# Kernel optimization log

Measured on AMD Instinct MI355X. Metric: run time of the kernel, lower is better.

The kernel has to match this reference:

```python
import jax, jax.numpy as jnp
import numpy as np
import math

NUM_BUCKETS = 32
MAX_DISTANCE = 128
N_HEADS = 16
D_KV = 64
D_MODEL = 1024


def _relative_position_bucket(relative_position, num_buckets=NUM_BUCKETS, max_distance=MAX_DISTANCE):
    # bidirectional (encoder) variant
    num_buckets = num_buckets // 2
    relative_buckets = (relative_position > 0).astype(jnp.int32) * num_buckets
    relative_position = jnp.abs(relative_position)
    max_exact = num_buckets // 2
    is_small = relative_position < max_exact
    # avoid log(0); masked by is_small anyway
    rp = jnp.maximum(relative_position, 1).astype(jnp.float32)
    rel_if_large = max_exact + (
        jnp.log(rp / max_exact) / math.log(max_distance / max_exact) * (num_buckets - max_exact)
    ).astype(jnp.int32)
    rel_if_large = jnp.minimum(rel_if_large, num_buckets - 1)
    relative_buckets = relative_buckets + jnp.where(is_small, relative_position, rel_if_large)
    return relative_buckets


def compute_bias(rel_bias, q_len, k_len):
    context = jnp.arange(q_len, dtype=jnp.int32)[:, None]
    memory = jnp.arange(k_len, dtype=jnp.int32)[None, :]
    buckets = _relative_position_bucket(memory - context)  # [q,k]
    values = rel_bias[buckets]                              # [q,k,H]
    return jnp.transpose(values, (2, 0, 1))[None]           # [1,H,q,k]


def setup_inputs() -> dict:
    key = jax.random.key(0)
    k1, k2, k3, k4 = jax.random.split(key, 4)
    B, S = 2, 2048
    hidden_states = jax.random.normal(k1, (B, S, D_MODEL), dtype=jnp.float32)
    attention_mask = jnp.ones((B, S), dtype=jnp.int32)
    w_qkv = jax.random.normal(k2, (3 * D_MODEL, D_MODEL), dtype=jnp.float32) * 0.02
    rel_bias = jax.random.normal(k3, (NUM_BUCKETS, N_HEADS), dtype=jnp.float32)
    w_o = jax.random.normal(k4, (D_MODEL, D_MODEL), dtype=jnp.float32) * 0.02
    return {"hidden_states": hidden_states, "attention_mask": attention_mask,
            "w_qkv": w_qkv, "rel_bias": rel_bias, "w_o": w_o}


def reference(hidden_states, attention_mask, w_qkv, rel_bias, w_o):
    B, S, _ = hidden_states.shape
    n, c = N_HEADS, D_KV
    qkv = hidden_states @ w_qkv.T                      # [B,S,3*inner]
    q, k, v = jnp.split(qkv, 3, axis=-1)
    q = q.reshape(B, S, n, c)
    k = k.reshape(B, S, n, c)
    v = v.reshape(B, S, n, c)
    attn_bias = jnp.broadcast_to(compute_bias(rel_bias, S, S), (B, n, S, S))
    mask = attention_mask.reshape(B, 1, 1, S)
    mask_val = jnp.finfo(q.dtype).min
    attn_bias = jnp.where(mask == 0, mask_val, attn_bias)
    attn = jnp.einsum('binc,bjnc->bnij', q, k) + attn_bias   # no 1/sqrt(d) scale in T5
    attn = jax.nn.softmax(attn.astype(jnp.float32), axis=-1).astype(q.dtype)
    x = jnp.einsum('bnij,bjnc->binc', attn, v)
    x = x.reshape(B, S, n * c)
    return x @ w_o.T
```

## Files before the change

### kernel.cpp

```cpp
#include <hip/hip_runtime.h>
#include <stdint.h>

typedef __attribute__((ext_vector_type(4))) float f32x4;
typedef __attribute__((ext_vector_type(8))) short short8;
typedef __attribute__((ext_vector_type(4))) short short4v;
typedef __attribute__((ext_vector_type(2))) unsigned uint2v;

__device__ __forceinline__ short f2bf(float f) {
    union { float f; unsigned u; } x; x.f = f;
    return (short)((x.u + 0x7fffu + ((x.u >> 16) & 1u)) >> 16);
}

__device__ __forceinline__ unsigned cvt_pk_bf16(float lo, float hi) {
    unsigned r;
    asm("v_cvt_pk_bf16_f32 %0, %1, %2" : "=v"(r) : "v"(lo), "v"(hi));
    return r;
}

__device__ __forceinline__ float fexp2(float x) {
#if __has_builtin(__builtin_amdgcn_exp2f)
    return __builtin_amdgcn_exp2f(x);
#else
    return exp2f(x);
#endif
}

#define MFMA16(a, b, c) __builtin_amdgcn_mfma_f32_16x16x32_bf16((a), (b), (c), 0, 0, 0)

__device__ __forceinline__ void gload16(const void* g, void* l) {
    __builtin_amdgcn_global_load_lds((const __attribute__((address_space(1))) void*)g,
                                     (__attribute__((address_space(3))) void*)l, 16, 0, 0);
}

__global__ __launch_bounds__(256) void cast_all(const float* __restrict__ h,
                                                const float* __restrict__ wq,
                                                const float* __restrict__ wo,
                                                short* __restrict__ hb,
                                                short* __restrict__ wqb,
                                                short* __restrict__ wob) {
    int i = blockIdx.x * 256 + threadIdx.x;
    const float* s;
    short* d;
    int j;
    if (i < 524288) { s = h; d = hb; j = i; }
    else if (i < 917504) { s = wq; d = wqb; j = i - 524288; }
    else { s = wo; d = wob; j = i - 917504; }
    float4 a = ((const float4*)s)[j * 2];
    float4 b = ((const float4*)s)[j * 2 + 1];
    short8 o;
    o[0] = f2bf(a.x); o[1] = f2bf(a.y); o[2] = f2bf(a.z); o[3] = f2bf(a.w);
    o[4] = f2bf(b.x); o[5] = f2bf(b.y); o[6] = f2bf(b.z); o[7] = f2bf(b.w);
    ((short8*)d)[j] = o;
}

template <int OUT_BF16, int QSCALE>
__global__ __launch_bounds__(512, 2) void gemm8p(const short* __restrict__ A,
                                                 const short* __restrict__ B,
                                                 void* __restrict__ Cout,
                                                 int M, int N, int K) {
    __shared__ short lds[2][4][8192];
    const int t = threadIdx.x;
    const int l = t & 63, w = t >> 6;
    const int lr = l & 15, lg = l >> 4;
    const int wr = w >> 2, wc = w & 3;
    const int m0 = blockIdx.y * 256, n0 = blockIdx.x * 256;
    const int nt = K >> 6, nh = nt << 2;

    const int sr0 = t >> 2;
    const int scc = ((t & 3) ^ ((sr0 >> 1) & 3)) * 8;
    const short* As0 = A + (size_t)(m0 + sr0) * K + scc;
    const short* As1 = A + (size_t)(m0 + sr0 + 128) * K + scc;
    const short* Bs0 = B + (size_t)(n0 + sr0) * K + scc;
    const short* Bs1 = B + (size_t)(n0 + sr0 + 128) * K + scc;
    short* ldsb = &lds[0][0][0];

    auto stageH = [&](int H) {
        int Tp = H >> 2, pos = H & 3;
        int kb = Tp * 64 + ((pos <= 1) ? 32 : 0);
        short* dst = ldsb + ((Tp & 1) * 4 + pos) * 8192 + t * 8;
        if (pos & 1) {
            gload16(As0 + kb, dst);
            gload16(As1 + kb, dst + 4096);
        } else {
            gload16(Bs0 + kb, dst);
            gload16(Bs1 + kb, dst + 4096);
        }
    };

    int aoff[8], boff[4];
    #pragma unroll
    for (int mi = 0; mi < 8; ++mi) {
        int row = wr * 128 + mi * 16 + lr;
        aoff[mi] = row * 32 + (lg ^ ((row >> 1) & 3)) * 8;
    }
    #pragma unroll
    for (int ni = 0; ni < 4; ++ni) {
        int row = wc * 64 + ni * 16 + lr;
        boff[ni] = row * 32 + (lg ^ ((row >> 1) & 3)) * 8;
    }

    f32x4 acc[8][4] = {};

    for (int H = 0; H < 7; ++H) stageH(H);
    asm volatile("s_waitcnt vmcnt(6)" ::: "memory");
    __builtin_amdgcn_s_barrier();

    for (int T = 0; T < nt; ++T) {
        const short* rbase = ldsb + (T & 1) * 32768;
        const short* B1b = rbase;
        const short* A1b = rbase + 8192;
        const short* B0b = rbase + 16384;
        const short* A0b = rbase + 24576;
        const int Hs = (T << 2) + 7;
        short8 a[4], b[4];

        #pragma unroll
        for (int i = 0; i < 4; ++i) a[i] = *(const short8*)(A1b + aoff[i]);
        #pragma unroll
        for (int i = 0; i < 4; ++i) b[i] = *(const short8*)(B1b + boff[i]);
        if (Hs < nh) stageH(Hs);
        __builtin_amdgcn_sched_barrier(0);
        __builtin_amdgcn_s_barrier();
        asm volatile("s_waitcnt lgkmcnt(0)" ::: "memory");
        __builtin_amdgcn_sched_barrier(0);
        __builtin_amdgcn_s_setprio(1);
        #pragma unroll
        for (int mi = 0; mi < 4; ++mi)
            #pragma unroll
            for (int ni = 0; ni < 4; ++ni)
                acc[mi][ni] = MFMA16(a[mi], b[ni], acc[mi][ni]);
        __builtin_amdgcn_s_setprio(0);
        __builtin_amdgcn_sched_barrier(0);
        __builtin_amdgcn_s_barrier();

        #pragma unroll
        for (int i = 0; i < 4; ++i) a[i] = *(const short8*)(A1b + aoff[4 + i]);
        if (Hs + 1 < nh) stageH(Hs + 1);
        __builtin_amdgcn_sched_barrier(0);
        __builtin_amdgcn_s_barrier();
        asm volatile("s_waitcnt lgkmcnt(0)" ::: "memory");
        __builtin_amdgcn_sched_barrier(0);
        __builtin_amdgcn_s_setprio(1);
        #pragma unroll
        for (int mi = 0; mi < 4; ++mi)
            #pragma unroll
            for (int ni = 0; ni < 4; ++ni)
                acc[4 + mi][ni] = MFMA16(a[mi], b[ni], acc[4 + mi][ni]);
        __builtin_amdgcn_s_setprio(0);
        __builtin_amdgcn_sched_barrier(0);
        __builtin_amdgcn_s_barrier();

        #pragma unroll
        for (int i = 0; i < 4; ++i) a[i] = *(const short8*)(A0b + aoff[i]);
        #pragma unroll
        for (int i = 0; i < 4; ++i) b[i] = *(const short8*)(B0b + boff[i]);
        if (Hs + 2 < nh) stageH(Hs + 2);
        __builtin_amdgcn_sched_barrier(0);
        __builtin_amdgcn_s_barrier();
        asm volatile("s_waitcnt lgkmcnt(0)" ::: "memory");
        __builtin_amdgcn_sched_barrier(0);
        __builtin_amdgcn_s_setprio(1);
        #pragma unroll
        for (int mi = 0; mi < 4; ++mi)
            #pragma unroll
            for (int ni = 0; ni < 4; ++ni)
                acc[mi][ni] = MFMA16(a[mi], b[ni], acc[mi][ni]);
        __builtin_amdgcn_s_setprio(0);
        __builtin_amdgcn_sched_barrier(0);
        __builtin_amdgcn_s_barrier();

        #pragma unroll
        for (int i = 0; i < 4; ++i) a[i] = *(const short8*)(A0b + aoff[4 + i]);
        if (Hs + 3 < nh) stageH(Hs + 3);
        __builtin_amdgcn_sched_barrier(0);
        __builtin_amdgcn_s_barrier();
        asm volatile("s_waitcnt lgkmcnt(0)" ::: "memory");
        __builtin_amdgcn_sched_barrier(0);
        __builtin_amdgcn_s_setprio(1);
        #pragma unroll
        for (int mi = 0; mi < 4; ++mi)
            #pragma unroll
            for (int ni = 0; ni < 4; ++ni)
                acc[4 + mi][ni] = MFMA16(a[mi], b[ni], acc[4 + mi][ni]);
        __builtin_amdgcn_s_setprio(0);
        if (T < nt - 2) {
            asm volatile("s_waitcnt vmcnt(6)" ::: "memory");
        } else if (T == nt - 2) {
            asm volatile("s_waitcnt vmcnt(0)" ::: "memory");
        }
        __builtin_amdgcn_sched_barrier(0);
        __builtin_amdgcn_s_barrier();
    }

    const float qs = (QSCALE && n0 < 1024) ? 1.4426950408889634f : 1.0f;
    #pragma unroll
    for (int mi = 0; mi < 8; ++mi)
        #pragma unroll
        for (int ni = 0; ni < 4; ++ni)
            #pragma unroll
            for (int rr = 0; rr < 4; ++rr) {
                int mm = m0 + wr * 128 + mi * 16 + lg * 4 + rr;
                int nn = n0 + wc * 64 + ni * 16 + lr;
                float v = acc[mi][ni][rr] * qs;
                if (OUT_BF16) ((short*)Cout)[(size_t)mm * N + nn] = f2bf(v);
                else ((float*)Cout)[(size_t)mm * N + nn] = v;
            }
}

template <int OUT_BF16, int QSCALE>
__global__ __launch_bounds__(256) void gemm_bt(const short* __restrict__ A,
                                               const short* __restrict__ B,
                                               void* __restrict__ Cout,
                                               int M, int N, int K) {
    __shared__ short sA[4096];
    __shared__ short sB[4096];
    const int t = threadIdx.x;
    const int l = t & 63, w = t >> 6;
    const int lr = l & 15, lg = l >> 4;
    const int m0 = blockIdx.y * 128, n0 = blockIdx.x * 128;
    const int wm = (w >> 1) * 64, wn = (w & 1) * 64;
    const int c0 = w * 64 + l, c1 = c0 + 256;
    const short* Ap0 = A + (size_t)(m0 + (c0 >> 2)) * K + (c0 & 3) * 8;
    const short* Ap1 = A + (size_t)(m0 + (c1 >> 2)) * K + (c1 & 3) * 8;
    const short* Bp0 = B + (size_t)(n0 + (c0 >> 2)) * K + (c0 & 3) * 8;
    const short* Bp1 = B + (size_t)(n0 + (c1 >> 2)) * K + (c1 & 3) * 8;
    short* lA0 = sA + w * 512;
    short* lA1 = sA + 2048 + w * 512;
    short* lB0 = sB + w * 512;
    short* lB1 = sB + 2048 + w * 512;
    f32x4 acc[4][4] = {};
    for (int k0 = 0; k0 < K; k0 += 32) {
        gload16(Ap0 + k0, lA0);
        gload16(Ap1 + k0, lA1);
        gload16(Bp0 + k0, lB0);
        gload16(Bp1 + k0, lB1);
        __syncthreads();
        short8 af[4], bfr[4];
        #pragma unroll
        for (int m = 0; m < 4; ++m) af[m] = *(const short8*)&sA[(wm + m * 16 + lr) * 32 + lg * 8];
        #pragma unroll
        for (int n = 0; n < 4; ++n) bfr[n] = *(const short8*)&sB[(wn + n * 16 + lr) * 32 + lg * 8];
        #pragma unroll
        for (int m = 0; m < 4; ++m)
            #pragma unroll
            for (int n = 0; n < 4; ++n)
                acc[m][n] = MFMA16(af[m], bfr[n], acc[m][n]);
        __syncthreads();
    }
    const float qs = (QSCALE && n0 < 1024) ? 1.4426950408889634f : 1.0f;
    #pragma unroll
    for (int m = 0; m < 4; ++m)
        #pragma unroll
        for (int n = 0; n < 4; ++n)
            #pragma unroll
            for (int r = 0; r < 4; ++r) {
                int mm = m0 + wm + m * 16 + lg * 4 + r;
                int nn = n0 + wn + n * 16 + lr;
                float v = acc[m][n][r] * qs;
                if (OUT_BF16) ((short*)Cout)[(size_t)mm * N + nn] = f2bf(v);
                else ((float*)Cout)[(size_t)mm * N + nn] = v;
            }
}

__global__ __launch_bounds__(256) void transpose_v(const short* __restrict__ qkv,
                                                   short* __restrict__ vt) {
    __shared__ short T[64][72];
    const int t = threadIdx.x;
    const int s0 = blockIdx.x * 64, bh = blockIdx.y;
    const int b = bh >> 4, h = bh & 15;
    const int rl = t >> 2, cg = (t & 3) * 16;
    const short* src = qkv + (size_t)(b * 2048 + s0 + rl) * 3072 + 2048 + h * 64 + cg;
    *(short8*)&T[rl][cg] = *(const short8*)src;
    *(short8*)&T[rl][cg + 8] = *(const short8*)(src + 8);
    __syncthreads();
    short8 o0, o1;
    #pragma unroll
    for (int e = 0; e < 8; ++e) o0[e] = T[cg + e][rl];
    #pragma unroll
    for (int e = 0; e < 8; ++e) o1[e] = T[cg + 8 + e][rl];
    short* dst = vt + ((size_t)bh * 64 + rl) * 2048 + s0 + cg;
    *(short8*)dst = o0;
    *(short8*)(dst + 8) = o1;
}

__global__ __launch_bounds__(256, 5) void attn_kernel(const short* __restrict__ qkv,
                                                      const short* __restrict__ vt,
                                                      const int* __restrict__ amask,
                                                      const float* __restrict__ rel_bias,
                                                      short* __restrict__ xout) {
    __shared__ float tbl[340];
    __shared__ short sK[4096];
    __shared__ short sV[4096];
    __shared__ short sP[4][16][72];
    __shared__ int mflags[32];
    const int t = threadIdx.x;
    const int l = t & 63, w = t >> 6;
    const int lr = l & 15, lg = l >> 4;
    const int qt = blockIdx.x, bh = blockIdx.y;
    const int b = bh >> 4, h = bh & 15;
    const int q0 = qt * 64 + w * 16;
    const float LOG2E = 1.4426950408889634f;

    if (t < 32) mflags[t] = ~0;
    for (int idx = t; idx < 337; idx += 256) {
        int d = idx - 168;
        int a = d < 0 ? -d : d;
        int fb = a < 8 ? a
                 : (a < 12 ? 8 : a < 16 ? 9 : a < 23 ? 10 : a < 32 ? 11
                    : a < 46 ? 12 : a < 64 ? 13 : a < 91 ? 14 : 15);
        int bk = (d > 0 ? 16 : 0) + fb;
        tbl[idx] = rel_bias[bk * 16 + h] * LOG2E;
    }
    const float rbp = rel_bias[31 * 16 + h] * LOG2E;
    const float rbn = rel_bias[15 * 16 + h] * LOG2E;

    short8 qf[2];
    #pragma unroll
    for (int ds = 0; ds < 2; ++ds)
        qf[ds] = *(const short8*)(qkv + (size_t)(b * 2048 + q0 + lr) * 3072 + h * 64 + ds * 32 + lg * 8);

    const int4* mq = (const int4*)(amask + b * 2048 + t * 8);
    int4 ma = mq[0], mb = mq[1];

    const int srow = t >> 3;
    const int scp = ((t & 7) ^ (srow & 7)) * 8;
    const short* kgp = qkv + (size_t)(b * 2048 + srow) * 3072 + 1024 + h * 64 + scp;
    const short* kgp2 = kgp + (size_t)32 * 3072;
    const short* vgp = vt + ((size_t)bh * 64 + srow) * 2048 + scp;
    const short* vgp2 = vgp + (size_t)32 * 2048;
    short* ldsK = sK + w * 512;
    short* ldsV = sV + w * 512;
    const int sw8 = (lr & 7) * 8;
    const int ibb = -q0 + lg * 4 - lr + 168;

    __syncthreads();
    int mok = ma.x & ma.y & ma.z & ma.w & mb.x & mb.y & mb.z & mb.w;
    if (mok == 0) atomicAnd(&mflags[t >> 3], 0);

    f32x4 o[4] = {};
    float mreg = -1e30f, lreg = 0.f;

    for (int kt = 0; kt < 2048; kt += 64) {
        gload16(kgp + (size_t)kt * 3072, ldsK);
        gload16(kgp2 + (size_t)kt * 3072, ldsK + 2048);
        gload16(vgp + kt, ldsV);
        gload16(vgp2 + kt, ldsV + 2048);
        __syncthreads();

        f32x4 pe[4];
        #pragma unroll
        for (int ct = 0; ct < 4; ++ct) {
            f32x4 z = {};
            #pragma unroll
            for (int ds = 0; ds < 2; ++ds) {
                short8 kf = *(const short8*)&sK[(ct * 16 + lr) * 64 + ((ds * 32 + lg * 8) ^ sw8)];
                z = MFMA16(kf, qf[ds], z);
            }
            pe[ct] = z;
        }

        float cb;
        if (kt >= q0 + 106) {
            cb = rbp;
        } else if (kt + 63 <= q0 - 91) {
            cb = rbn;
        } else {
            cb = 0.f;
            const int ib = kt + ibb;
            #pragma unroll
            for (int ct = 0; ct < 4; ++ct)
                #pragma unroll
                for (int r = 0; r < 4; ++r)
                    pe[ct][r] += tbl[ib + ct * 16 + r];
        }

        float t0 = fmaxf(fmaxf(pe[0][0], pe[0][1]), fmaxf(pe[0][2], pe[0][3]));
        float t1 = fmaxf(fmaxf(pe[1][0], pe[1][1]), fmaxf(pe[1][2], pe[1][3]));
        float t2 = fmaxf(fmaxf(pe[2][0], pe[2][1]), fmaxf(pe[2][2], pe[2][3]));
        float t3 = fmaxf(fmaxf(pe[3][0], pe[3][1]), fmaxf(pe[3][2], pe[3][3]));
        float lmax = fmaxf(fmaxf(t0, t1), fmaxf(t2, t3));
        if (__any(lmax > mreg - cb + 11.5f)) {
            float rm = fmaxf(lmax, __shfl_xor(lmax, 16));
            rm = fmaxf(rm, __shfl_xor(rm, 32));
            float mnew = fmaxf(mreg, rm + cb);
            float alpha = fexp2(mreg - mnew);
            lreg *= alpha;
            #pragma unroll
            for (int dt = 0; dt < 4; ++dt)
                #pragma unroll
                for (int r = 0; r < 4; ++r)
                    o[dt][r] *= alpha;
            mreg = mnew;
        }
        const float madj = mreg - cb;
        const int tok = mflags[kt >> 6];
        float rs = 0.f;
        if (tok) {
            #pragma unroll
            for (int ct = 0; ct < 4; ++ct) {
                float p[4];
                #pragma unroll
                for (int r = 0; r < 4; ++r) {
                    float pv = fexp2(pe[ct][r] - madj);
                    p[r] = pv;
                    rs += pv;
                }
                uint2v pk;
                pk[0] = cvt_pk_bf16(p[0], p[1]);
                pk[1] = cvt_pk_bf16(p[2], p[3]);
                *(uint2v*)&sP[w][lr][ct * 16 + lg * 4] = pk;
            }
        } else {
            const int4* mp = (const int4*)(amask + b * 2048 + kt);
            #pragma unroll
            for (int ct = 0; ct < 4; ++ct) {
                int4 cm = mp[ct * 4 + lg];
                float p[4];
                #pragma unroll
                for (int r = 0; r < 4; ++r) {
                    float pv = fexp2(pe[ct][r] - madj);
                    pv = ((const int*)&cm)[r] ? pv : 0.f;
                    p[r] = pv;
                    rs += pv;
                }
                uint2v pk;
                pk[0] = cvt_pk_bf16(p[0], p[1]);
                pk[1] = cvt_pk_bf16(p[2], p[3]);
                *(uint2v*)&sP[w][lr][ct * 16 + lg * 4] = pk;
            }
        }
        lreg += rs;

        #pragma unroll
        for (int kk = 0; kk < 2; ++kk) {
            short8 pf = *(const short8*)&sP[w][lr][kk * 32 + lg * 8];
            #pragma unroll
            for (int dt = 0; dt < 4; ++dt) {
                short8 vf = *(const short8*)&sV[(dt * 16 + lr) * 64 + ((kk * 32 + lg * 8) ^ sw8)];
                o[dt] = MFMA16(vf, pf, o[dt]);
            }
        }
        __syncthreads();
    }

    float lsum = lreg + __shfl_xor(lreg, 16);
    lsum += __shfl_xor(lsum, 32);
    const float inv = 1.0f / lsum;
    #pragma unroll
    for (int dt = 0; dt < 4; ++dt) {
        short4v ov;
        #pragma unroll
        for (int r = 0; r < 4; ++r) ov[r] = f2bf(o[dt][r] * inv);
        *(short4v*)(xout + (size_t)(b * 2048 + q0 + lr) * 1024 + h * 64 + dt * 16 + lg * 4) = ov;
    }
}

extern "C" void kernel_launch(void* const* d_in, const int* in_sizes, int n_in,
                              void* d_out, int out_size, void* d_ws, size_t ws_size,
                              hipStream_t stream) {
    const float* hidden = (const float*)d_in[0];
    const int* amask = (const int*)d_in[1];
    const float* w_qkv = (const float*)d_in[2];
    const float* rel_bias = (const float*)d_in[3];
    const float* w_o = (const float*)d_in[4];
    if (ws_size < 58720256) return;
    char* ws = (char*)d_ws;
    short* hidden_bf = (short*)(ws + 0);
    short* wqkv_bf   = (short*)(ws + 8388608);
    short* wo_bf     = (short*)(ws + 14680064);
    short* qkv       = (short*)(ws + 16777216);
    short* vt        = (short*)(ws + 41943040);
    short* xbuf      = (short*)(ws + 50331648);

    cast_all<<<4096, 256, 0, stream>>>(hidden, w_qkv, w_o, hidden_bf, wqkv_bf, wo_bf);
    gemm8p<1, 1><<<dim3(12, 16), 512, 0, stream>>>(hidden_bf, wqkv_bf, qkv, 4096, 3072, 1024);
    transpose_v<<<dim3(32, 32), 256, 0, stream>>>(qkv, vt);
    attn_kernel<<<dim3(32, 32), 256, 0, stream>>>(qkv, vt, amask, rel_bias, xbuf);
    gemm_bt<0, 0><<<dim3(8, 32), 256, 0, stream>>>(xbuf, wo_bf, d_out, 4096, 1024, 1024);
}
```

Measured before the change: 138.9 us.

## Double-buffer K/V tiles in LDS to overlap global loads with compute

Splits the K and V LDS buffers in two so the next tile is prefetched with async global-to-LDS loads while the current tile is processed, using explicit vmcnt waits and raw barriers. This targets the load latency that the single-buffered loop exposed at every iteration. It doubles the K/V shared memory and lowers launch_bounds occupancy from 5 to 3 blocks per CU, which reduces latency hiding through wave parallelism.

```diff
diff --git a/kernel.cpp b/kernel.cpp
--- a/kernel.cpp
+++ b/kernel.cpp
@@ -283,14 +283,14 @@
     *(short8*)(dst + 8) = o1;
 }
 
-__global__ __launch_bounds__(256, 5) void attn_kernel(const short* __restrict__ qkv,
+__global__ __launch_bounds__(256, 3) void attn_kernel(const short* __restrict__ qkv,
                                                       const short* __restrict__ vt,
                                                       const int* __restrict__ amask,
                                                       const float* __restrict__ rel_bias,
                                                       short* __restrict__ xout) {
     __shared__ float tbl[340];
-    __shared__ short sK[4096];
-    __shared__ short sV[4096];
+    __shared__ short sK[2][4096];
+    __shared__ short sV[2][4096];
     __shared__ short sP[4][16][72];
     __shared__ int mflags[32];
     const int t = threadIdx.x;
@@ -328,24 +328,42 @@
     const short* kgp2 = kgp + (size_t)32 * 3072;
     const short* vgp = vt + ((size_t)bh * 64 + srow) * 2048 + scp;
     const short* vgp2 = vgp + (size_t)32 * 2048;
-    short* ldsK = sK + w * 512;
-    short* ldsV = sV + w * 512;
     const int sw8 = (lr & 7) * 8;
     const int ibb = -q0 + lg * 4 - lr + 168;
 
     __syncthreads();
     int mok = ma.x & ma.y & ma.z & ma.w & mb.x & mb.y & mb.z & mb.w;
     if (mok == 0) atomicAnd(&mflags[t >> 3], 0);
+    __syncthreads();
+
+    gload16(kgp, &sK[0][0] + w * 512);
+    gload16(kgp2, &sK[0][0] + 2048 + w * 512);
+    gload16(vgp, &sV[0][0] + w * 512);
+    gload16(vgp2, &sV[0][0] + 2048 + w * 512);
 
     f32x4 o[4] = {};
     float mreg = -1e30f, lreg = 0.f;
 
     for (int kt = 0; kt < 2048; kt += 64) {
-        gload16(kgp + (size_t)kt * 3072, ldsK);
-        gload16(kgp2 + (size_t)kt * 3072, ldsK + 2048);
-        gload16(vgp + kt, ldsV);
-        gload16(vgp2 + kt, ldsV + 2048);
-        __syncthreads();
+        const int cur = (kt >> 6) & 1;
+        const bool more = (kt + 64 < 2048);
+        if (more) {
+            short* nk = &sK[cur ^ 1][0];
+            short* nv = &sV[cur ^ 1][0];
+            gload16(kgp + (size_t)(kt + 64) * 3072, nk + w * 512);
+            gload16(kgp2 + (size_t)(kt + 64) * 3072, nk + 2048 + w * 512);
+            gload16(vgp + kt + 64, nv + w * 512);
+            gload16(vgp2 + kt + 64, nv + 2048 + w * 512);
+            asm volatile("s_waitcnt vmcnt(4)" ::: "memory");
+        } else {
+            asm volatile("s_waitcnt vmcnt(0)" ::: "memory");
+        }
+        __builtin_amdgcn_sched_barrier(0);
+        __builtin_amdgcn_s_barrier();
+        __builtin_amdgcn_sched_barrier(0);
+
+        const short* kb = &sK[cur][0];
+        const short* vb = &sV[cur][0];
 
         f32x4 pe[4];
         #pragma unroll
@@ -353,7 +371,7 @@
             f32x4 z = {};
             #pragma unroll
             for (int ds = 0; ds < 2; ++ds) {
-                short8 kf = *(const short8*)&sK[(ct * 16 + lr) * 64 + ((ds * 32 + lg * 8) ^ sw8)];
+                short8 kf = *(const short8*)&kb[(ct * 16 + lr) * 64 + ((ds * 32 + lg * 8) ^ sw8)];
                 z = MFMA16(kf, qf[ds], z);
             }
             pe[ct] = z;
@@ -436,11 +454,13 @@
             short8 pf = *(const short8*)&sP[w][lr][kk * 32 + lg * 8];
             #pragma unroll
             for (int dt = 0; dt < 4; ++dt) {
-                short8 vf = *(const short8*)&sV[(dt * 16 + lr) * 64 + ((kk * 32 + lg * 8) ^ sw8)];
+                short8 vf = *(const short8*)&vb[(dt * 16 + lr) * 64 + ((kk * 32 + lg * 8) ^ sw8)];
                 o[dt] = MFMA16(vf, pf, o[dt]);
             }
         }
-        __syncthreads();
+        __builtin_amdgcn_sched_barrier(0);
+        __builtin_amdgcn_s_barrier();
+        __builtin_amdgcn_sched_barrier(0);
     }
 
     float lsum = lreg + __shfl_xor(lreg, 16);
```

Result: slower. 156.0 us (+12.3%).
